# Kernel optimization log

Measured on AMD Instinct MI355X. Metric: run time of the kernel, lower is better.

The kernel has to match this reference:

```python
import jax, jax.numpy as jnp
import numpy as np

B, N, D, H = 2, 4096, 512, 8
HD = D // H

def setup_inputs() -> dict:
    key = jax.random.key(0)
    ks = jax.random.split(key, 5)
    s = 1.0 / np.sqrt(D)
    return {
        "x": jax.random.normal(ks[0], (B, N, D), dtype=jnp.float32),
        "W_qkv": jax.random.uniform(ks[1], (D, 3 * D), minval=-s, maxval=s, dtype=jnp.float32),
        "b_qkv": jax.random.uniform(ks[2], (3 * D,), minval=-s, maxval=s, dtype=jnp.float32),
        "W_out": jax.random.uniform(ks[3], (D, D), minval=-s, maxval=s, dtype=jnp.float32),
        "b_out": jax.random.uniform(ks[4], (D,), minval=-s, maxval=s, dtype=jnp.float32),
    }

def reference(x, W_qkv, b_qkv, W_out, b_out):
    Bq, Nq, Dq = x.shape
    scale = HD ** -0.5
    qkv = x @ W_qkv + b_qkv                      # [B,N,3D]
    qkv = qkv.reshape(Bq, Nq, 3, H, HD)
    q, k, v = (jnp.moveaxis(qkv[:, :, i], 2, 1) for i in range(3))  # [B,H,N,hd]
    attn = jnp.einsum('bhqd,bhkd->bhqk', q, k) * scale   # [B,H,N,N]
    causal = jnp.tril(jnp.ones((Nq, Nq), dtype=bool))
    attn = jnp.where(causal, attn, -jnp.inf)
    attn = jax.nn.softmax(attn, axis=-1)
    out = jnp.einsum('bhqk,bhkd->bhqd', attn, v)         # [B,H,N,hd]
    out = jnp.moveaxis(out, 1, 2).reshape(Bq, Nq, Dq)
    return out @ W_out + b_out
```

## Files before the change

kernel.cpp:

```cpp
#include <hip/hip_runtime.h>
#include <hip/hip_bf16.h>


typedef __bf16 bf16_t;
typedef __bf16 bf16x2 __attribute__((ext_vector_type(2)));
typedef __bf16 bf16x4 __attribute__((ext_vector_type(4)));
typedef __bf16 bf16x8 __attribute__((ext_vector_type(8)));
typedef float  f32x4  __attribute__((ext_vector_type(4)));
typedef unsigned int uint32x4 __attribute__((ext_vector_type(4)));

__device__ __forceinline__ void gload_lds16(const bf16_t* g, bf16_t* l) {
    __builtin_amdgcn_global_load_lds(
        (const __attribute__((address_space(1))) void*)g,
        (__attribute__((address_space(3))) void*)l, 16, 0, 0);
}


__global__ void convert_f32_bf16(const float* __restrict__ in, bf16_t* __restrict__ out) {
    int i = blockIdx.x * 256 + threadIdx.x;
    float4 v = ((const float4*)in)[i];
    bf16x4 o;
    o[0] = (bf16_t)v.x; o[1] = (bf16_t)v.y; o[2] = (bf16_t)v.z; o[3] = (bf16_t)v.w;
    ((bf16x4*)out)[i] = o;
}

__global__ void transpose_tiled(const float* __restrict__ in, bf16_t* __restrict__ out, int N) {
    __shared__ bf16_t T[64][72];
    const int tid = threadIdx.x;
    const int n0 = blockIdx.x * 64, k0 = blockIdx.y * 64;
    #pragma unroll
    for (int pass = 0; pass < 4; ++pass) {
        int kk = pass * 16 + (tid >> 4), nn = (tid & 15) * 4;
        float4 v = *(const float4*)(in + (size_t)(k0 + kk) * N + n0 + nn);
        T[nn + 0][kk] = (bf16_t)v.x; T[nn + 1][kk] = (bf16_t)v.y;
        T[nn + 2][kk] = (bf16_t)v.z; T[nn + 3][kk] = (bf16_t)v.w;
    }
    __syncthreads();
    #pragma unroll
    for (int pass = 0; pass < 2; ++pass) {
        int n = pass * 32 + (tid >> 3), c8 = (tid & 7) * 8;
        *(bf16x8*)(out + (size_t)(n0 + n) * 512 + k0 + c8) = *(const bf16x8*)&T[n][c8];
    }
}

__global__ void transpose_v(const bf16_t* __restrict__ Vg, bf16_t* __restrict__ Vt) {
    __shared__ bf16_t T[64 * 64];
    const int tid = threadIdx.x;
    const int bh = blockIdx.x >> 6, n0 = (blockIdx.x & 63) * 64;
    const bf16_t* src = Vg + ((size_t)bh * 4096 + n0) * 64;
    #pragma unroll
    for (int i = 0; i < 2; ++i) {
        int c = tid + i * 256, n = c >> 3, h8 = (c & 7) * 8;
        bf16x8 v = *(const bf16x8*)(src + (size_t)n * 64 + h8);
        const int swz = (n >> 3) ^ (h8 >> 3);
        bf16_t* base = &T[swz * 8 + (n & 7)];
        #pragma unroll
        for (int j = 0; j < 8; ++j) base[(h8 + j) * 64] = v[j];
    }
    __syncthreads();
    bf16_t* dst = Vt + (size_t)bh * 64 * 4096 + n0;
    #pragma unroll
    for (int i = 0; i < 2; ++i) {
        int c = tid + i * 256, hd = c >> 3, cn = c & 7;
        *(bf16x8*)(dst + (size_t)hd * 4096 + cn * 8) =
            *(const bf16x8*)&T[hd * 64 + ((cn ^ (hd >> 3)) * 8)];
    }
}


template <int MODE, int TN>
__global__ __launch_bounds__(256) void gemm_bt(
    const bf16_t* __restrict__ A, const bf16_t* __restrict__ Bt,
    const float* __restrict__ bias,
    bf16_t* __restrict__ Qg, bf16_t* __restrict__ Kg, bf16_t* __restrict__ Vg,
    float* __restrict__ Cout)
{
    constexpr int NI = (TN == 128) ? 4 : 2;
    __shared__ bf16_t As[128 * 64];
    __shared__ bf16_t Bs[TN * 64];
    const int tid  = threadIdx.x;
    const int wid  = tid >> 6, lane = tid & 63, l16 = lane & 15, quad = lane >> 4;
    const int l8   = l16 & 7;
    const int wr   = (TN == 128) ? (wid >> 1) * 64 : wid * 32;
    const int wc   = (TN == 128) ? (wid & 1) * 64 : 0;
    const int m0   = blockIdx.y * 128, n0 = blockIdx.x * TN;

    f32x4 acc[NI][4] = {};

    for (int kk = 0; kk < 512; kk += 64) {
        __syncthreads();
        #pragma unroll
        for (int i = 0; i < 4; ++i) {
            int slot = tid + i * 256;
            int row = slot >> 3, cg = (slot & 7) ^ (row & 7);
            gload_lds16(A + (size_t)(m0 + row) * 512 + kk + cg * 8,
                        (bf16_t*)((char*)As + ((i * 256 + (wid << 6)) << 4)));
        }
        #pragma unroll
        for (int i = 0; i < TN / 32; ++i) {
            int slot = tid + i * 256;
            int row = slot >> 3, cg = (slot & 7) ^ (row & 7);
            gload_lds16(Bt + (size_t)(n0 + row) * 512 + kk + cg * 8,
                        (bf16_t*)((char*)Bs + ((i * 256 + (wid << 6)) << 4)));
        }
        __syncthreads();
        #pragma unroll
        for (int s = 0; s < 2; ++s) {
            const int sw = (s * 4 + quad);
            bf16x8 a[NI], b[4];
            #pragma unroll
            for (int i = 0; i < NI; ++i) {
                int row = wr + i * 16 + l16;
                a[i] = *(const bf16x8*)&As[(row * 8 + (sw ^ l8)) * 8];
            }
            #pragma unroll
            for (int j = 0; j < 4; ++j) {
                int row = wc + j * 16 + l16;
                b[j] = *(const bf16x8*)&Bs[(row * 8 + (sw ^ l8)) * 8];
            }
            #pragma unroll
            for (int i = 0; i < NI; ++i)
                #pragma unroll
                for (int j = 0; j < 4; ++j)
                    acc[i][j] = __builtin_amdgcn_mfma_f32_16x16x32_bf16(a[i], b[j], acc[i][j], 0, 0, 0);
        }
    }

    const float qscale = 0.18033688011112042f;
    #pragma unroll
    for (int i = 0; i < NI; ++i) {
        int mrow = m0 + wr + i * 16 + quad * 4;
        #pragma unroll
        for (int j = 0; j < 4; ++j) {
            int cgl = n0 + wc + j * 16 + l16;
            float bv = bias[cgl];
            #pragma unroll
            for (int r = 0; r < 4; ++r) {
                int m = mrow + r;
                float val = acc[i][j][r] + bv;
                if (MODE == 0) {
                    int which = cgl >> 9, hh = (cgl >> 6) & 7, hd = cgl & 63;
                    int b_ = m >> 12, n = m & 4095, bh = b_ * 8 + hh;
                    size_t idx = ((size_t)bh * 4096 + n) * 64 + hd;
                    if (which == 0)      Qg[idx] = (bf16_t)(val * qscale);
                    else if (which == 1) Kg[idx] = (bf16_t)val;
                    else                 Vg[idx] = (bf16_t)val;
                } else {
                    Cout[(size_t)m * 512 + cgl] = val;
                }
            }
        }
    }
}


__global__ __launch_bounds__(256, 2) void attn_ns2(
    const bf16_t* __restrict__ Qg, const bf16_t* __restrict__ Kg,
    const bf16_t* __restrict__ Vt,
    float* __restrict__ o_part, float* __restrict__ l_part, int nsplit)
{
    __shared__ bf16_t Ks[2][64][72];
    __shared__ bf16_t Vs[2][64][72];

    const int tid  = threadIdx.x;
    const int w    = tid >> 6, lane = tid & 63, l16 = lane & 15, quad = lane >> 4;
    const int bh   = blockIdx.x & 15, pr = (blockIdx.x >> 4) & 7, h = blockIdx.x >> 7;

    float* ob = o_part + (size_t)(h * 16 + bh) * 4096 * 64;
    float* lb = l_part + (size_t)(h * 16 + bh) * 4096;

    const int srow = tid >> 3, scol = (tid & 7) * 8;
    const int srow1 = srow + 32;
    const float MSHIFT = 12.0f;

    bf16x8 ones;
    #pragma unroll
    for (int j = 0; j < 8; ++j) ones[j] = (bf16_t)1.0f;

    uint4 kr0, kr1, vr0, vr1;

    for (int ph = 0; ph < 2; ++ph) {
        const int st = ph ? (15 - pr) : pr;
        const int T  = 4 * st + 4;
        const int b0 = (h * T) / nsplit, b1 = ((h + 1) * T) / nsplit;

        int qrow[4];
        bf16x8 qf[4][2];
        #pragma unroll
        for (int s = 0; s < 4; ++s) {
            qrow[s] = st * 256 + s * 64 + w * 16 + l16;
            const bf16_t* qp = Qg + ((size_t)bh * 4096 + qrow[s]) * 64;
            qf[s][0] = *(const bf16x8*)(qp + quad * 8);
            qf[s][1] = *(const bf16x8*)(qp + 32 + quad * 8);
        }

        f32x4 o[4][4] = {};
        f32x4 lacc[4] = {};

        {
            const size_t kb = ((size_t)bh * 4096 + b0 * 64) * 64;
            const size_t vb = (size_t)bh * 64 * 4096 + b0 * 64;
            kr0 = *(const uint4*)(Kg + kb + (size_t)srow * 64 + scol);
            kr1 = *(const uint4*)(Kg + kb + (size_t)srow1 * 64 + scol);
            vr0 = *(const uint4*)(Vt + vb + (size_t)srow * 4096 + scol);
            vr1 = *(const uint4*)(Vt + vb + (size_t)srow1 * 4096 + scol);
        }
        __syncthreads();

        for (int kt = b0; kt < b1; ++kt) {
            const int cur = kt & 1;
            *(uint4*)&Ks[cur][srow][scol]  = kr0;
            *(uint4*)&Ks[cur][srow1][scol] = kr1;
            *(uint4*)&Vs[cur][srow][scol]  = vr0;
            *(uint4*)&Vs[cur][srow1][scol] = vr1;
            __syncthreads();

            if (kt + 1 < b1) {
                const size_t kb = ((size_t)bh * 4096 + (kt + 1) * 64) * 64;
                const size_t vb = (size_t)bh * 64 * 4096 + (kt + 1) * 64;
                kr0 = *(const uint4*)(Kg + kb + (size_t)srow * 64 + scol);
                kr1 = *(const uint4*)(Kg + kb + (size_t)srow1 * 64 + scol);
                vr0 = *(const uint4*)(Vt + vb + (size_t)srow * 4096 + scol);
                vr1 = *(const uint4*)(Vt + vb + (size_t)srow1 * 4096 + scol);
            }

            bf16x8 kf[4][2], vf[4][2];
            #pragma unroll
            for (int cb = 0; cb < 4; ++cb) {
                kf[cb][0] = *(const bf16x8*)&Ks[cur][cb * 16 + l16][quad * 8];
                kf[cb][1] = *(const bf16x8*)&Ks[cur][cb * 16 + l16][32 + quad * 8];
            }
            #pragma unroll
            for (int j = 0; j < 4; ++j) {
                vf[j][0] = *(const bf16x8*)&Vs[cur][j * 16 + l16][quad * 8];
                vf[j][1] = *(const bf16x8*)&Vs[cur][j * 16 + l16][32 + quad * 8];
            }

            #pragma unroll
            for (int s = 0; s < 4; ++s) {
                const int diag = 4 * st + s;
                if (kt > diag) continue;

                f32x4 sv[4] = {};
                #pragma unroll
                for (int cb = 0; cb < 4; ++cb) {
                    sv[cb] = __builtin_amdgcn_mfma_f32_16x16x32_bf16(kf[cb][0], qf[s][0], sv[cb], 0, 0, 0);
                    sv[cb] = __builtin_amdgcn_mfma_f32_16x16x32_bf16(kf[cb][1], qf[s][1], sv[cb], 0, 0, 0);
                }

                if (kt == diag) {
                    #pragma unroll
                    for (int cb = 0; cb < 4; ++cb) {
                        const int keyg = kt * 64 + cb * 16 + quad * 4;
                        #pragma unroll
                        for (int r = 0; r < 4; ++r)
                            if (keyg + r > qrow[s]) sv[cb][r] = -1e30f;
                    }
                }

                unsigned int c[4][2];
                #pragma unroll
                for (int cb = 0; cb < 4; ++cb) {
                    #pragma unroll
                    for (int t = 0; t < 2; ++t) {
                        bf16x2 pk2;
                        pk2[0] = (bf16_t)__builtin_amdgcn_exp2f(sv[cb][2 * t]     - MSHIFT);
                        pk2[1] = (bf16_t)__builtin_amdgcn_exp2f(sv[cb][2 * t + 1] - MSHIFT);
                        c[cb][t] = __builtin_bit_cast(unsigned int, pk2);
                    }
                }

                unsigned int pw0[4], pw1[4];
                #pragma unroll
                for (int t = 0; t < 2; ++t) {
                    auto u  = __builtin_amdgcn_permlane32_swap(c[0][t], c[1][t], false, false);
                    auto z  = __builtin_amdgcn_permlane16_swap(u[0], u[1], false, false);
                    pw0[t] = z[0]; pw0[t + 2] = z[1];
                    auto u2 = __builtin_amdgcn_permlane32_swap(c[2][t], c[3][t], false, false);
                    auto z2 = __builtin_amdgcn_permlane16_swap(u2[0], u2[1], false, false);
                    pw1[t] = z2[0]; pw1[t + 2] = z2[1];
                }
                uint32x4 w0v = {pw0[0], pw0[1], pw0[2], pw0[3]};
                uint32x4 w1v = {pw1[0], pw1[1], pw1[2], pw1[3]};
                bf16x8 pa0 = __builtin_bit_cast(bf16x8, w0v);
                bf16x8 pa1 = __builtin_bit_cast(bf16x8, w1v);

                #pragma unroll
                for (int j = 0; j < 4; ++j) {
                    o[s][j] = __builtin_amdgcn_mfma_f32_16x16x32_bf16(pa0, vf[j][0], o[s][j], 0, 0, 0);
                    o[s][j] = __builtin_amdgcn_mfma_f32_16x16x32_bf16(pa1, vf[j][1], o[s][j], 0, 0, 0);
                }
                lacc[s] = __builtin_amdgcn_mfma_f32_16x16x32_bf16(pa0, ones, lacc[s], 0, 0, 0);
                lacc[s] = __builtin_amdgcn_mfma_f32_16x16x32_bf16(pa1, ones, lacc[s], 0, 0, 0);
            }
        }

        #pragma unroll
        for (int s = 0; s < 4; ++s)
            #pragma unroll
            for (int r = 0; r < 4; ++r) {
                int n = st * 256 + s * 64 + w * 16 + quad * 4 + r;
                #pragma unroll
                for (int j = 0; j < 4; ++j)
                    ob[(size_t)n * 64 + j * 16 + l16] = o[s][j][r];
                if (l16 == 0) lb[n] = lacc[s][r];
            }
    }
}

__global__ void combine_kernel(const float* __restrict__ o_part,
                               const float* __restrict__ l_part,
                               bf16_t* __restrict__ Og, int ns)
{
    int t = blockIdx.x * 256 + threadIdx.x;
    int oct = t & 7, n = (t >> 3) & 4095, bh = t >> 15;
    size_t base = ((size_t)bh * 4096 + n) * 64 + oct * 8;
    f32x4 s0 = {}, s1 = {};
    float l = 0.f;
    for (int h = 0; h < ns; ++h) {
        const float* op = o_part + (size_t)h * 16 * 4096 * 64 + base;
        s0 += *(const f32x4*)op;
        s1 += *(const f32x4*)(op + 4);
        l  += l_part[(size_t)h * 16 * 4096 + (size_t)bh * 4096 + n];
    }
    float inv = 1.0f / l;
    bf16x8 res;
    #pragma unroll
    for (int j = 0; j < 4; ++j) {
        res[j]     = (bf16_t)(s0[j] * inv);
        res[j + 4] = (bf16_t)(s1[j] * inv);
    }
    *(bf16x8*)(Og + ((size_t)((bh >> 3) * 4096 + n)) * 512 + (bh & 7) * 64 + oct * 8) = res;
}


extern "C" void kernel_launch(void* const* d_in, const int* in_sizes, int n_in,
                              void* d_out, int out_size, void* d_ws, size_t ws_size,
                              hipStream_t stream) {
    const float* x    = (const float*)d_in[0];
    const float* Wqkv = (const float*)d_in[1];
    const float* bqkv = (const float*)d_in[2];
    const float* Wout = (const float*)d_in[3];
    const float* bout = (const float*)d_in[4];
    float* out = (float*)d_out;

    char* ws = (char*)d_ws;
    bf16_t* xb  = (bf16_t*)(ws);
    bf16_t* WqT = (bf16_t*)(ws + 8388608);
    bf16_t* WoT = (bf16_t*)(ws + 9961472);
    bf16_t* Qg  = (bf16_t*)(ws + 10485760);
    bf16_t* Kg  = (bf16_t*)(ws + 18874368);
    bf16_t* Vt  = (bf16_t*)(ws + 27262976);
    bf16_t* Vg  = (bf16_t*)(ws + 35651584);

    const int nsplit = (ws_size >= 103809024ULL) ? 4
                     : (ws_size >= 86769664ULL)  ? 3 : 2;
    float* o_part = (float*)(ws + 35651584);
    float* l_part = (float*)(ws + 35651584 + (size_t)nsplit * 16777216);

    convert_f32_bf16<<<4096, 256, 0, stream>>>(x, xb);
    transpose_tiled<<<dim3(24, 8), 256, 0, stream>>>(Wqkv, WqT, 1536);
    transpose_tiled<<<dim3(8, 8), 256, 0, stream>>>(Wout, WoT, 512);

    gemm_bt<0, 128><<<dim3(12, 64), 256, 0, stream>>>(xb, WqT, bqkv, Qg, Kg, Vg, nullptr);
    transpose_v<<<1024, 256, 0, stream>>>(Vg, Vt);

    attn_ns2<<<128 * nsplit, 256, 0, stream>>>(Qg, Kg, Vt, o_part, l_part, nsplit);
    combine_kernel<<<2048, 256, 0, stream>>>(o_part, l_part, xb , nsplit);

    gemm_bt<1, 64><<<dim3(8, 64), 256, 0, stream>>>(xb, WoT, bout, nullptr, nullptr, nullptr, out);
}
```

Before: 182.9 us.

## Fuse V transpose into QKV GEMM epilogue via swizzled LDS staging

The QKV GEMM epilogue now stages the output tile in shared memory with an XOR swizzle. It then writes Q and K as vectorized 16-byte rows and writes V directly in transposed layout. This removes the separate transpose_v kernel launch and its extra global read and write of V, and replaces scattered 2-byte epilogue stores with coalesced vector stores. The cost is extra LDS traffic, two more barriers in the epilogue, and gather-style 2-byte LDS reads for the V transpose path.

```diff
diff --git a/kernel.cpp b/kernel.cpp
--- a/kernel.cpp
+++ b/kernel.cpp
@@ -43,41 +43,18 @@
     }
 }
 
-__global__ void transpose_v(const bf16_t* __restrict__ Vg, bf16_t* __restrict__ Vt) {
-    __shared__ bf16_t T[64 * 64];
-    const int tid = threadIdx.x;
-    const int bh = blockIdx.x >> 6, n0 = (blockIdx.x & 63) * 64;
-    const bf16_t* src = Vg + ((size_t)bh * 4096 + n0) * 64;
-    #pragma unroll
-    for (int i = 0; i < 2; ++i) {
-        int c = tid + i * 256, n = c >> 3, h8 = (c & 7) * 8;
-        bf16x8 v = *(const bf16x8*)(src + (size_t)n * 64 + h8);
-        const int swz = (n >> 3) ^ (h8 >> 3);
-        bf16_t* base = &T[swz * 8 + (n & 7)];
-        #pragma unroll
-        for (int j = 0; j < 8; ++j) base[(h8 + j) * 64] = v[j];
-    }
-    __syncthreads();
-    bf16_t* dst = Vt + (size_t)bh * 64 * 4096 + n0;
-    #pragma unroll
-    for (int i = 0; i < 2; ++i) {
-        int c = tid + i * 256, hd = c >> 3, cn = c & 7;
-        *(bf16x8*)(dst + (size_t)hd * 4096 + cn * 8) =
-            *(const bf16x8*)&T[hd * 64 + ((cn ^ (hd >> 3)) * 8)];
-    }
-}
-
 
 template <int MODE, int TN>
 __global__ __launch_bounds__(256) void gemm_bt(
     const bf16_t* __restrict__ A, const bf16_t* __restrict__ Bt,
     const float* __restrict__ bias,
-    bf16_t* __restrict__ Qg, bf16_t* __restrict__ Kg, bf16_t* __restrict__ Vg,
+    bf16_t* __restrict__ Qg, bf16_t* __restrict__ Kg, bf16_t* __restrict__ Vtp,
     float* __restrict__ Cout)
 {
     constexpr int NI = (TN == 128) ? 4 : 2;
-    __shared__ bf16_t As[128 * 64];
-    __shared__ bf16_t Bs[TN * 64];
+    __shared__ bf16_t smem[128 * 64 + TN * 64];
+    bf16_t* As = smem;
+    bf16_t* Bs = smem + 128 * 64;
     const int tid  = threadIdx.x;
     const int wid  = tid >> 6, lane = tid & 63, l16 = lane & 15, quad = lane >> 4;
     const int l8   = l16 & 7;
@@ -127,26 +104,75 @@
     }
 
     const float qscale = 0.18033688011112042f;
-    #pragma unroll
-    for (int i = 0; i < NI; ++i) {
-        int mrow = m0 + wr + i * 16 + quad * 4;
-        #pragma unroll
-        for (int j = 0; j < 4; ++j) {
-            int cgl = n0 + wc + j * 16 + l16;
-            float bv = bias[cgl];
-            #pragma unroll
-            for (int r = 0; r < 4; ++r) {
-                int m = mrow + r;
-                float val = acc[i][j][r] + bv;
-                if (MODE == 0) {
-                    int which = cgl >> 9, hh = (cgl >> 6) & 7, hd = cgl & 63;
-                    int b_ = m >> 12, n = m & 4095, bh = b_ * 8 + hh;
-                    size_t idx = ((size_t)bh * 4096 + n) * 64 + hd;
-                    if (which == 0)      Qg[idx] = (bf16_t)(val * qscale);
-                    else if (which == 1) Kg[idx] = (bf16_t)val;
-                    else                 Vg[idx] = (bf16_t)val;
-                } else {
-                    Cout[(size_t)m * 512 + cgl] = val;
+
+    if (MODE == 0) {
+        __syncthreads();
+        bf16_t* E = smem;
+        const float qs = (n0 < 512) ? qscale : 1.0f;
+        #pragma unroll
+        for (int i = 0; i < NI; ++i) {
+            #pragma unroll
+            for (int j = 0; j < 4; ++j) {
+                int col = wc + j * 16 + l16;
+                float bv = bias[n0 + col];
+                #pragma unroll
+                for (int r = 0; r < 4; ++r) {
+                    int row = wr + i * 16 + quad * 4 + r;
+                    int sc = (((col >> 3) ^ (row & 15) ^ ((row >> 3) & 7)) << 3) + (col & 7);
+                    E[row * 128 + sc] = (bf16_t)((acc[i][j][r] + bv) * qs);
+                }
+            }
+        }
+        __syncthreads();
+
+        const int b_ = m0 >> 12;
+        if (n0 < 1024) {
+            bf16_t* dst = (n0 < 512) ? Qg : Kg;
+            #pragma unroll
+            for (int p = 0; p < 8; ++p) {
+                int g = p * 256 + tid;
+                int c = g & 7, drow = g >> 3;
+                int hsel = drow >> 7, nl = drow & 127;
+                int col0 = hsel * 64 + c * 8;
+                int sc = (((col0 >> 3) ^ (nl & 15) ^ ((nl >> 3) & 7)) << 3);
+                bf16x8 v = *(const bf16x8*)&E[nl * 128 + sc];
+                int hh = ((n0 + hsel * 64) >> 6) & 7;
+                int n = (m0 & 4095) + nl;
+                size_t idx = (((size_t)(b_ * 8 + hh) * 4096) + n) * 64 + c * 8;
+                *(bf16x8*)(dst + idx) = v;
+            }
+        } else {
+            #pragma unroll
+            for (int p = 0; p < 8; ++p) {
+                int g = p * 256 + tid;
+                int cn8 = g & 15, hdrow = g >> 4;
+                int hsel = hdrow >> 6, hd = hdrow & 63;
+                int col = hsel * 64 + hd;
+                bf16x8 v;
+                #pragma unroll
+                for (int k = 0; k < 8; ++k) {
+                    int row = cn8 * 8 + k;
+                    int sc = (((col >> 3) ^ (row & 15) ^ ((row >> 3) & 7)) << 3) + (col & 7);
+                    v[k] = E[row * 128 + sc];
+                }
+                int hh = ((n0 + hsel * 64) >> 6) & 7;
+                int nbase = (m0 & 4095) + cn8 * 8;
+                size_t idx = ((size_t)(b_ * 8 + hh) * 64 + hd) * 4096 + nbase;
+                *(bf16x8*)(Vtp + idx) = v;
+            }
+        }
+    } else {
+        #pragma unroll
+        for (int i = 0; i < NI; ++i) {
+            int mrow = m0 + wr + i * 16 + quad * 4;
+            #pragma unroll
+            for (int j = 0; j < 4; ++j) {
+                int cgl = n0 + wc + j * 16 + l16;
+                float bv = bias[cgl];
+                #pragma unroll
+                for (int r = 0; r < 4; ++r) {
+                    int m = mrow + r;
+                    Cout[(size_t)m * 512 + cgl] = acc[i][j][r] + bv;
                 }
             }
         }
@@ -351,7 +377,6 @@
     bf16_t* Qg  = (bf16_t*)(ws + 10485760);
     bf16_t* Kg  = (bf16_t*)(ws + 18874368);
     bf16_t* Vt  = (bf16_t*)(ws + 27262976);
-    bf16_t* Vg  = (bf16_t*)(ws + 35651584);
 
     const int nsplit = (ws_size >= 103809024ULL) ? 4
                      : (ws_size >= 86769664ULL)  ? 3 : 2;
@@ -362,8 +387,7 @@
     transpose_tiled<<<dim3(24, 8), 256, 0, stream>>>(Wqkv, WqT, 1536);
     transpose_tiled<<<dim3(8, 8), 256, 0, stream>>>(Wout, WoT, 512);
 
-    gemm_bt<0, 128><<<dim3(12, 64), 256, 0, stream>>>(xb, WqT, bqkv, Qg, Kg, Vg, nullptr);
-    transpose_v<<<1024, 256, 0, stream>>>(Vg, Vt);
+    gemm_bt<0, 128><<<dim3(12, 64), 256, 0, stream>>>(xb, WqT, bqkv, Qg, Kg, Vt, nullptr);
 
     attn_ns2<<<128 * nsplit, 256, 0, stream>>>(Qg, Kg, Vt, o_part, l_part, nsplit);
     combine_kernel<<<2048, 256, 0, stream>>>(o_part, l_part, xb , nsplit);
```

After: 180.9 us. Within noise of the previous version (-1.1%).
